# Performance work log

Measured on AMD Instinct MI355X. Metric: run time of the kernel, lower is better.

The kernel has to match this reference:

```python
import jax, jax.numpy as jnp
import numpy as np

N_NODES = 50000
N_EDGES = 320000
D_IN = 256
D_OUT = 256


def setup_inputs() -> dict:
    key = jax.random.key(0)
    k1, k2, k3, k4, k5, k6, k7 = jax.random.split(key, 7)
    s = 1.0 / np.sqrt(D_IN)
    return {
        "node_features": jax.random.normal(k1, (N_NODES, D_IN), dtype=jnp.float32),
        "edge_index": jax.random.randint(k2, (2, N_EDGES), 0, N_NODES, dtype=jnp.int64),
        "w1": jax.random.uniform(k3, (D_OUT, D_IN), jnp.float32, -s, s),
        "w2": jax.random.uniform(k4, (D_OUT, D_IN), jnp.float32, -s, s),
        "w3": jax.random.uniform(k5, (D_OUT, D_IN), jnp.float32, -s, s),
        "b3": jax.random.uniform(k6, (D_OUT,), jnp.float32, -s, s),
    }


def reference(node_features, edge_index, w1, w2, w3, b3):
    # GraphSAGE-style conv: project, gather messages from senders,
    # scatter-sum at receivers, project, combine with self term.
    n = node_features.shape[0]
    proj = node_features @ w3.T + b3                 # [N, D_OUT]
    msgs = proj[edge_index[0]]                       # [E, D_OUT] gather senders
    agg = jax.ops.segment_sum(msgs, edge_index[1], num_segments=n)  # [N, D_OUT]
    out = node_features @ w1.T + agg @ w2.T          # [N, D_OUT]
    return out
```

## Files before the change

### kernel.cpp

```cpp
#include <hip/hip_runtime.h>

#define NN 50000
#define NPAD 50048
#define NE 320000
#define D 256
#define CAP 64
#define NCSR 1250
#define NCONV 6250

typedef __bf16 bf16x8 __attribute__((ext_vector_type(8)));
typedef float f32x4 __attribute__((ext_vector_type(4)));

__device__ __forceinline__ unsigned short f2bf(float f) {
    unsigned u = __builtin_bit_cast(unsigned, f);
    unsigned r = u + 0x7FFFu + ((u >> 16) & 1u);
    return (unsigned short)(r >> 16);
}
__device__ __forceinline__ float bflo(unsigned u) {
    return __builtin_bit_cast(float, u << 16);
}
__device__ __forceinline__ float bfhi(unsigned u) {
    return __builtin_bit_cast(float, u & 0xFFFF0000u);
}
__device__ __forceinline__ unsigned packbf(float lo, float hi) {
    return (unsigned)f2bf(lo) | ((unsigned)f2bf(hi) << 16);
}

__global__ __launch_bounds__(256) void prep_weights(
        const float* __restrict__ w1, const float* __restrict__ w2,
        const float* __restrict__ w3, const float* __restrict__ b3,
        unsigned short* __restrict__ WTT, float* __restrict__ bvec,
        int* __restrict__ cnt) {
    const int j = blockIdx.x;
    const int k = threadIdx.x;
    const int g = j * 256 + k;
    if (g < NN) cnt[g] = 0;
    __shared__ float w2row[D];
    __shared__ float red[D];
    w2row[k] = w2[j * D + k];
    __syncthreads();
    float acc = 0.f;
    #pragma unroll 8
    for (int o = 0; o < D; ++o) acc += w2row[o] * w3[o * D + k];
    WTT[(size_t)j * 512 + k]     = f2bf(w1[j * D + k]);
    WTT[(size_t)j * 512 + D + k] = f2bf(acc);
    red[k] = w2row[k] * b3[k];
    __syncthreads();
    for (int s = 128; s > 0; s >>= 1) {
        if (k < s) red[k] += red[k + s];
        __syncthreads();
    }
    if (k == 0) bvec[j] = red[0];
}

__global__ __launch_bounds__(256) void convert_and_csr(
        const float* __restrict__ x, unsigned short* __restrict__ xbf,
        const int* __restrict__ ei, int* __restrict__ csr, int* __restrict__ cnt) {
    const int b = blockIdx.x;
    if (b < NCSR) {
        const int e = b * 256 + threadIdx.x;
        if (e < NE) {
            const int src = ei[e];
            const int dst = ei[NE + e];
            const int pos = atomicAdd(cnt + dst, 1);
            if (pos < CAP) csr[(size_t)dst * CAP + pos] = src;
        }
    } else {
        const size_t i = ((size_t)(b - NCSR) * 256 + threadIdx.x) * 8;
        const float4 a0 = *reinterpret_cast<const float4*>(x + i);
        const float4 a1 = *reinterpret_cast<const float4*>(x + i + 4);
        ushort4 o0 = {f2bf(a0.x), f2bf(a0.y), f2bf(a0.z), f2bf(a0.w)};
        ushort4 o1 = {f2bf(a1.x), f2bf(a1.y), f2bf(a1.z), f2bf(a1.w)};
        *reinterpret_cast<ushort4*>(xbf + i)     = o0;
        *reinterpret_cast<ushort4*>(xbf + i + 4) = o1;
    }
}

__global__ __launch_bounds__(256) void agg_gather(
        const unsigned short* __restrict__ xbf, const int* __restrict__ csr,
        const int* __restrict__ cnt, unsigned short* __restrict__ aggbf) {
    const int node = blockIdx.x * 8 + (threadIdx.x >> 5);
    const int l32  = threadIdx.x & 31;
    if (node >= NN) return;
    int d = cnt[node]; if (d > CAP) d = CAP;
    const int* __restrict__ row = csr + (size_t)node * CAP;
    const int d32 = d < 32 ? d : 32;
    int v = (l32 < d32) ? row[l32] : 0x7FFFFFFF;
    #pragma unroll
    for (int k = 2; k <= 32; k <<= 1) {
        #pragma unroll
        for (int j = k >> 1; j > 0; j >>= 1) {
            const int o = __shfl_xor(v, j, 32);
            const int lo = v < o ? v : o;
            const int hi = v < o ? o : v;
            const bool dir   = (l32 & k) == 0;
            const bool lower = (l32 & j) == 0;
            v = (dir == lower) ? lo : hi;
        }
    }
    float a0 = 0.f, a1 = 0.f, a2 = 0.f, a3 = 0.f;
    float a4 = 0.f, a5 = 0.f, a6 = 0.f, a7 = 0.f;
    int i = 0;
    for (; i + 4 <= d32; i += 4) {
        const int s0 = __shfl(v, i,     32);
        const int s1 = __shfl(v, i + 1, 32);
        const int s2 = __shfl(v, i + 2, 32);
        const int s3 = __shfl(v, i + 3, 32);
        const uint4 p = *reinterpret_cast<const uint4*>(xbf + (size_t)s0 * D + l32 * 8);
        const uint4 q = *reinterpret_cast<const uint4*>(xbf + (size_t)s1 * D + l32 * 8);
        const uint4 u = *reinterpret_cast<const uint4*>(xbf + (size_t)s2 * D + l32 * 8);
        const uint4 t = *reinterpret_cast<const uint4*>(xbf + (size_t)s3 * D + l32 * 8);
        a0 += (bflo(p.x) + bflo(q.x)) + (bflo(u.x) + bflo(t.x));
        a1 += (bfhi(p.x) + bfhi(q.x)) + (bfhi(u.x) + bfhi(t.x));
        a2 += (bflo(p.y) + bflo(q.y)) + (bflo(u.y) + bflo(t.y));
        a3 += (bfhi(p.y) + bfhi(q.y)) + (bfhi(u.y) + bfhi(t.y));
        a4 += (bflo(p.z) + bflo(q.z)) + (bflo(u.z) + bflo(t.z));
        a5 += (bfhi(p.z) + bfhi(q.z)) + (bfhi(u.z) + bfhi(t.z));
        a6 += (bflo(p.w) + bflo(q.w)) + (bflo(u.w) + bflo(t.w));
        a7 += (bfhi(p.w) + bfhi(q.w)) + (bfhi(u.w) + bfhi(t.w));
    }
    for (; i < d32; ++i) {
        const int s = __shfl(v, i, 32);
        const uint4 p = *reinterpret_cast<const uint4*>(xbf + (size_t)s * D + l32 * 8);
        a0 += bflo(p.x); a1 += bfhi(p.x);
        a2 += bflo(p.y); a3 += bfhi(p.y);
        a4 += bflo(p.z); a5 += bfhi(p.z);
        a6 += bflo(p.w); a7 += bfhi(p.w);
    }
    for (; i < d; ++i) {
        const uint4 p = *reinterpret_cast<const uint4*>(xbf + (size_t)row[i] * D + l32 * 8);
        a0 += bflo(p.x); a1 += bfhi(p.x);
        a2 += bflo(p.y); a3 += bfhi(p.y);
        a4 += bflo(p.z); a5 += bfhi(p.z);
        a6 += bflo(p.w); a7 += bfhi(p.w);
    }
    uint4 o = {packbf(a0, a1), packbf(a2, a3), packbf(a4, a5), packbf(a6, a7)};
    *reinterpret_cast<uint4*>(aggbf + (size_t)node * D + l32 * 8) = o;
}

__global__ __launch_bounds__(256) void gemm_tiled(
        const unsigned short* __restrict__ xbf, const unsigned short* __restrict__ aggbf,
        const unsigned short* __restrict__ WTT, const float* __restrict__ bvec,
        const int* __restrict__ cnt, float* __restrict__ out) {
    __shared__ __align__(16) unsigned char smem[24576];
    unsigned short* ldsA = (unsigned short*)smem;
    unsigned short* ldsB = (unsigned short*)(smem + 8192);

    const int nwg = gridDim.x;
    const int q   = nwg >> 3, r = nwg & 7;
    const int xcd = blockIdx.x & 7, pos = blockIdx.x >> 3;
    const int wg  = (xcd < r ? xcd * (q + 1) : r * (q + 1) + (xcd - r) * q) + pos;

    const int tid  = threadIdx.x;
    const int w    = tid >> 6;
    const int lane = tid & 63;
    const int l16  = lane & 15;
    const int g4   = lane >> 4;
    const int wm   = w >> 1, wn = w & 1;
    const int gr0  = (wg >> 1) * 64;
    const int nb0  = (wg & 1) * 128;

    f32x4 acc[2][4];
    #pragma unroll
    for (int a = 0; a < 2; ++a)
        #pragma unroll
        for (int b = 0; b < 4; ++b) acc[a][b] = (f32x4)0.f;

    for (int kt = 0; kt < 8; ++kt) {
        if (kt) __syncthreads();
        {
            const unsigned short* __restrict__ srcA = (kt < 4) ? xbf : aggbf;
            const int kcA = (kt & 3) * 64;
            #pragma unroll
            for (int p = 0; p < 2; ++p) {
                const int idx = p * 256 + w * 64 + lane;
                const int rr = idx >> 3, c = idx & 7;
                const int sw = (c ^ (rr & 7)) << 3;
                const unsigned short* gp = srcA + ((size_t)(gr0 + rr) << 8) + kcA + sw;
                unsigned short* lp = ldsA + ((p * 256 + w * 64) << 3);
                __builtin_amdgcn_global_load_lds(
                    (const __attribute__((address_space(1))) void*)(const void*)gp,
                    (__attribute__((address_space(3))) void*)(void*)lp, 16, 0, 0);
            }
            const int kcB = kt * 64;
            #pragma unroll
            for (int p = 0; p < 4; ++p) {
                const int idx = p * 256 + w * 64 + lane;
                const int rr = idx >> 3, c = idx & 7;
                const int sw = (c ^ (rr & 7)) << 3;
                const unsigned short* gp = WTT + ((size_t)(nb0 + rr) << 9) + kcB + sw;
                unsigned short* lp = ldsB + ((p * 256 + w * 64) << 3);
                __builtin_amdgcn_global_load_lds(
                    (const __attribute__((address_space(1))) void*)(const void*)gp,
                    (__attribute__((address_space(3))) void*)(void*)lp, 16, 0, 0);
            }
        }
        __syncthreads();

        #pragma unroll
        for (int kh = 0; kh < 2; ++kh) {
            const int cb = kh * 4 + g4;
            bf16x8 af[2], bfr[4];
            #pragma unroll
            for (int f = 0; f < 2; ++f) {
                const int ra = wm * 32 + f * 16 + l16;
                af[f] = *reinterpret_cast<const bf16x8*>(
                    ldsA + (ra * 8 + (cb ^ (ra & 7))) * 8);
            }
            #pragma unroll
            for (int f = 0; f < 4; ++f) {
                const int rb = wn * 64 + f * 16 + l16;
                bfr[f] = *reinterpret_cast<const bf16x8*>(
                    ldsB + (rb * 8 + (cb ^ (rb & 7))) * 8);
            }
            #pragma unroll
            for (int fm = 0; fm < 2; ++fm)
                #pragma unroll
                for (int fn = 0; fn < 4; ++fn)
                    acc[fm][fn] = __builtin_amdgcn_mfma_f32_16x16x32_bf16(
                        af[fm], bfr[fn], acc[fm][fn], 0, 0, 0);
        }
    }

    float* O = (float*)smem;
    #pragma unroll
    for (int half = 0; half < 2; ++half) {
        __syncthreads();
        if (wm == half) {
            #pragma unroll
            for (int fm = 0; fm < 2; ++fm)
                #pragma unroll
                for (int i = 0; i < 4; ++i) {
                    const int lr = fm * 16 + g4 * 4 + i;
                    float* po = O + lr * 132 + wn * 64 + l16;
                    #pragma unroll
                    for (int fn = 0; fn < 4; ++fn) po[fn * 16] = acc[fm][fn][i];
                }
        }
        __syncthreads();
        #pragma unroll
        for (int p = 0; p < 4; ++p) {
            const int id = tid + p * 256;
            const int rr = id >> 5;
            const int c4 = (id & 31) << 2;
            const int row = gr0 + half * 32 + rr;
            if (row < NN) {
                const float dg = (float)cnt[row];
                const float4 bv = *reinterpret_cast<const float4*>(bvec + nb0 + c4);
                float4 vv = *reinterpret_cast<const float4*>(O + rr * 132 + c4);
                vv.x += dg * bv.x; vv.y += dg * bv.y;
                vv.z += dg * bv.z; vv.w += dg * bv.w;
                *reinterpret_cast<float4*>(out + ((size_t)row << 8) + nb0 + c4) = vv;
            }
        }
    }
}

extern "C" void kernel_launch(void* const* d_in, const int* in_sizes, int n_in,
                              void* d_out, int out_size, void* d_ws, size_t ws_size,
                              hipStream_t stream) {
    const float* x  = (const float*)d_in[0];
    const int*   ei = (const int*)d_in[1];
    const float* w1 = (const float*)d_in[2];
    const float* w2 = (const float*)d_in[3];
    const float* w3 = (const float*)d_in[4];
    const float* b3 = (const float*)d_in[5];
    float* out = (float*)d_out;

    unsigned short* xbf   = (unsigned short*)d_ws;
    unsigned short* aggbf = xbf + (size_t)NPAD * D;
    unsigned short* WTT   = aggbf + (size_t)NPAD * D;
    float* bvec = (float*)(WTT + (size_t)D * 512);
    int*   cnt  = (int*)(bvec + D);
    int*   csr  = cnt + NN;

    prep_weights<<<D, 256, 0, stream>>>(w1, w2, w3, b3, WTT, bvec, cnt);
    convert_and_csr<<<NCSR + NCONV, 256, 0, stream>>>(x, xbf, ei, csr, cnt);
    agg_gather<<<(NN + 7) / 8, 256, 0, stream>>>(xbf, csr, cnt, aggbf);
    gemm_tiled<<<(NPAD / 64) * 2, 256, 0, stream>>>(xbf, aggbf, WTT, bvec, cnt, out);
}
```

Baseline: 97.13 us.

## Widen GEMM block to full 256 output columns with 512 threads

Each GEMM workgroup now computes a 64x256 output tile using 8 waves, instead of two workgroups each computing 64x128 with 4 waves. The A tiles (node features and aggregated features) are therefore loaded from global memory once per row block rather than once per column half. The XCD-aware block remapping is dropped since the column pairing no longer exists. In exchange, LDS use grows to 40 KB per block for the full B tile, which may reduce occupancy, and the epilogue is staged in two column halves.

```diff
diff --git a/kernel.cpp b/kernel.cpp
--- a/kernel.cpp
+++ b/kernel.cpp
@@ -138,27 +138,22 @@
     *reinterpret_cast<uint4*>(aggbf + (size_t)node * D + l32 * 8) = o;
 }
 
-__global__ __launch_bounds__(256) void gemm_tiled(
+__global__ __launch_bounds__(512) void gemm_tiled(
         const unsigned short* __restrict__ xbf, const unsigned short* __restrict__ aggbf,
         const unsigned short* __restrict__ WTT, const float* __restrict__ bvec,
         const int* __restrict__ cnt, float* __restrict__ out) {
-    __shared__ __align__(16) unsigned char smem[24576];
+    __shared__ __align__(16) unsigned char smem[40960];
     unsigned short* ldsA = (unsigned short*)smem;
     unsigned short* ldsB = (unsigned short*)(smem + 8192);
-
-    const int nwg = gridDim.x;
-    const int q   = nwg >> 3, r = nwg & 7;
-    const int xcd = blockIdx.x & 7, pos = blockIdx.x >> 3;
-    const int wg  = (xcd < r ? xcd * (q + 1) : r * (q + 1) + (xcd - r) * q) + pos;
 
     const int tid  = threadIdx.x;
     const int w    = tid >> 6;
     const int lane = tid & 63;
     const int l16  = lane & 15;
     const int g4   = lane >> 4;
-    const int wm   = w >> 1, wn = w & 1;
-    const int gr0  = (wg >> 1) * 64;
-    const int nb0  = (wg & 1) * 128;
+    const int wm   = w >> 2;
+    const int wn   = w & 3;
+    const int gr0  = blockIdx.x * 64;
 
     f32x4 acc[2][4];
     #pragma unroll
@@ -171,13 +166,12 @@
         {
             const unsigned short* __restrict__ srcA = (kt < 4) ? xbf : aggbf;
             const int kcA = (kt & 3) * 64;
-            #pragma unroll
-            for (int p = 0; p < 2; ++p) {
-                const int idx = p * 256 + w * 64 + lane;
+            {
+                const int idx = tid;
                 const int rr = idx >> 3, c = idx & 7;
                 const int sw = (c ^ (rr & 7)) << 3;
                 const unsigned short* gp = srcA + ((size_t)(gr0 + rr) << 8) + kcA + sw;
-                unsigned short* lp = ldsA + ((p * 256 + w * 64) << 3);
+                unsigned short* lp = ldsA + (idx << 3);
                 __builtin_amdgcn_global_load_lds(
                     (const __attribute__((address_space(1))) void*)(const void*)gp,
                     (__attribute__((address_space(3))) void*)(void*)lp, 16, 0, 0);
@@ -185,11 +179,11 @@
             const int kcB = kt * 64;
             #pragma unroll
             for (int p = 0; p < 4; ++p) {
-                const int idx = p * 256 + w * 64 + lane;
+                const int idx = p * 512 + tid;
                 const int rr = idx >> 3, c = idx & 7;
                 const int sw = (c ^ (rr & 7)) << 3;
-                const unsigned short* gp = WTT + ((size_t)(nb0 + rr) << 9) + kcB + sw;
-                unsigned short* lp = ldsB + ((p * 256 + w * 64) << 3);
+                const unsigned short* gp = WTT + ((size_t)rr << 9) + kcB + sw;
+                unsigned short* lp = ldsB + (idx << 3);
                 __builtin_amdgcn_global_load_lds(
                     (const __attribute__((address_space(1))) void*)(const void*)gp,
                     (__attribute__((address_space(3))) void*)(void*)lp, 16, 0, 0);
@@ -205,13 +199,13 @@
             for (int f = 0; f < 2; ++f) {
                 const int ra = wm * 32 + f * 16 + l16;
                 af[f] = *reinterpret_cast<const bf16x8*>(
-                    ldsA + (ra * 8 + (cb ^ (ra & 7))) * 8);
+                    ldsA + ((ra << 3) + (cb ^ (ra & 7))) * 8);
             }
             #pragma unroll
             for (int f = 0; f < 4; ++f) {
                 const int rb = wn * 64 + f * 16 + l16;
                 bfr[f] = *reinterpret_cast<const bf16x8*>(
-                    ldsB + (rb * 8 + (cb ^ (rb & 7))) * 8);
+                    ldsB + ((rb << 3) + (cb ^ (rb & 7))) * 8);
             }
             #pragma unroll
             for (int fm = 0; fm < 2; ++fm)
@@ -224,15 +218,15 @@
 
     float* O = (float*)smem;
     #pragma unroll
-    for (int half = 0; half < 2; ++half) {
-        __syncthreads();
-        if (wm == half) {
+    for (int h = 0; h < 2; ++h) {
+        __syncthreads();
+        if ((wn >> 1) == h) {
             #pragma unroll
             for (int fm = 0; fm < 2; ++fm)
                 #pragma unroll
                 for (int i = 0; i < 4; ++i) {
-                    const int lr = fm * 16 + g4 * 4 + i;
-                    float* po = O + lr * 132 + wn * 64 + l16;
+                    const int lr = wm * 32 + fm * 16 + g4 * 4 + i;
+                    float* po = O + lr * 132 + (wn & 1) * 64 + l16;
                     #pragma unroll
                     for (int fn = 0; fn < 4; ++fn) po[fn * 16] = acc[fm][fn][i];
                 }
@@ -240,17 +234,17 @@
         __syncthreads();
         #pragma unroll
         for (int p = 0; p < 4; ++p) {
-            const int id = tid + p * 256;
+            const int id = tid + p * 512;
             const int rr = id >> 5;
             const int c4 = (id & 31) << 2;
-            const int row = gr0 + half * 32 + rr;
+            const int row = gr0 + rr;
             if (row < NN) {
                 const float dg = (float)cnt[row];
-                const float4 bv = *reinterpret_cast<const float4*>(bvec + nb0 + c4);
+                const float4 bv = *reinterpret_cast<const float4*>(bvec + h * 128 + c4);
                 float4 vv = *reinterpret_cast<const float4*>(O + rr * 132 + c4);
                 vv.x += dg * bv.x; vv.y += dg * bv.y;
                 vv.z += dg * bv.z; vv.w += dg * bv.w;
-                *reinterpret_cast<float4*>(out + ((size_t)row << 8) + nb0 + c4) = vv;
+                *reinterpret_cast<float4*>(out + ((size_t)row << 8) + h * 128 + c4) = vv;
             }
         }
     }
@@ -277,5 +271,5 @@
     prep_weights<<<D, 256, 0, stream>>>(w1, w2, w3, b3, WTT, bvec, cnt);
     convert_and_csr<<<NCSR + NCONV, 256, 0, stream>>>(x, xbf, ei, csr, cnt);
     agg_gather<<<(NN + 7) / 8, 256, 0, stream>>>(xbf, csr, cnt, aggbf);
-    gemm_tiled<<<(NPAD / 64) * 2, 256, 0, stream>>>(xbf, aggbf, WTT, bvec, cnt, out);
-}
+    gemm_tiled<<<NPAD / 64, 512, 0, stream>>>(xbf, aggbf, WTT, bvec, cnt, out);
+}
```

Result: slower. 99.68 us (+2.6%).
